# Performance work log

Measured on AMD Instinct MI355X. Metric: run time of the kernel, lower is better.

Reference implementation:

```python
import jax, jax.numpy as jnp
import numpy as np

N_USERS = 50000
N_ITEMS = 50000
N = N_USERS + N_ITEMS
DIM = 64
N_LAYERS = 3
N_EDGES = 1250000
BN_EPS = 1e-5


def setup_inputs() -> dict:
    key = jax.random.key(0)
    k_x, k_e, k_w, k_b = jax.random.split(key, 4)
    x = jax.random.normal(k_x, (N, DIM), dtype=jnp.float32)
    edge_index = jax.random.randint(k_e, (2, N_EDGES), 0, N, dtype=jnp.int64)
    # Glorot-ish init for the per-layer GCNConv linear weights [L, DIM, DIM]
    Ws = jax.random.normal(k_w, (N_LAYERS, DIM, DIM), dtype=jnp.float32) * (1.0 / np.sqrt(DIM))
    bs = jnp.zeros((N_LAYERS, DIM), dtype=jnp.float32)
    gamma = jnp.ones((DIM,), dtype=jnp.float32)
    beta = jnp.zeros((DIM,), dtype=jnp.float32)
    return {"x": x, "edge_index": edge_index, "Ws": Ws, "bs": bs,
            "gamma": gamma, "beta": beta}


def _gcn_conv(x, W, b, src, dst, deg_inv_sqrt):
    # PyG GCNConv: h = x @ W^T ; out_i = sum_{j->i} norm_ji * h_j + b
    h = x @ W.T                                   # [N, DIM]
    norm = deg_inv_sqrt[src] * deg_inv_sqrt[dst]  # [E2]
    msg = h[src] * norm[:, None]                  # gather over irregular edges
    out = jax.ops.segment_sum(msg, dst, num_segments=N)
    return out + b


def reference(x, edge_index, Ws, bs, gamma, beta):
    # Add self-loops once (same augmented graph for every layer).
    loops = jnp.arange(N, dtype=edge_index.dtype)
    src = jnp.concatenate([edge_index[0], loops])  # source nodes j
    dst = jnp.concatenate([edge_index[1], loops])  # target nodes i
    # Symmetric normalization degrees (edge weight 1, counted at targets).
    deg = jax.ops.segment_sum(jnp.ones_like(dst, dtype=x.dtype), dst, num_segments=N)
    deg_inv_sqrt = jnp.where(deg > 0, jax.lax.rsqrt(deg), 0.0)

    for i in range(N_LAYERS):
        x = _gcn_conv(x, Ws[i], bs[i], src, dst, deg_inv_sqrt)

    # BatchNorm1d (training-mode batch statistics, biased variance)
    mean = jnp.mean(x, axis=0)
    var = jnp.mean((x - mean) ** 2, axis=0)
    x = (x - mean) * jax.lax.rsqrt(var + BN_EPS) * gamma + beta

    users, items = x[:N_USERS], x[N_USERS:]
    return users, items
```

## Files before the change

### kernel.cpp

```cpp
#include <hip/hip_runtime.h>

#define NN      100000
#define NUSERS  50000
#define NE      1250000
#define DIM     64
#define BN_EPS  1e-5f
#define NBUCK   8
#define NCHUNK  320
#define SLOT    40

typedef __attribute__((ext_vector_type(8))) short s16x8;
typedef __attribute__((ext_vector_type(4))) float f32x4;

__device__ __forceinline__ short f2b(float f) {
    unsigned u = __builtin_bit_cast(unsigned, f);
    u = (u + 0x7fffu + ((u >> 16) & 1u)) >> 16;
    return (short)u;
}
__device__ __forceinline__ float b2f(unsigned short s) {
    unsigned u = ((unsigned)s) << 16;
    return __builtin_bit_cast(float, u);
}

__global__ __launch_bounds__(256) void place_part(const int* __restrict__ ei,
                                                  int* __restrict__ cursor,
                                                  int* __restrict__ csr_src) {
    __shared__ int Qd[4][128];
    __shared__ int Qs[4][128];
    int lane = threadIdx.x & 63, wave = threadIdx.x >> 6;
    int B = blockIdx.x & (NBUCK - 1);
    int gw = (blockIdx.x >> 3) * 4 + wave;
    const int NW  = NCHUNK * 4;
    const int per = (NE + NW - 1) / NW;
    int e0 = gw * per;
    int e1 = e0 + per; if (e1 > NE) e1 = NE;
    int qn = 0;
    for (int e = e0 + lane; e - lane < e1; e += 64) {
        bool keep = false; int d = 0, s = 0;
        if (e < e1) {
            d = __builtin_nontemporal_load(&ei[NE + e]);
            keep = ((d / 12500) == B);
            if (keep) s = __builtin_nontemporal_load(&ei[e]);
        }
        unsigned long long m = __ballot(keep);
        if (keep) {
            int rank = __popcll(m & ((1ull << lane) - 1ull));
            Qd[wave][qn + rank] = d;
            Qs[wave][qn + rank] = s;
        }
        qn += __popcll(m);
        if (qn >= 64) {
            int dd = Qd[wave][lane];
            int ss = Qs[wave][lane];
            int pos = atomicAdd(&cursor[dd], 1);
            if (pos < SLOT) csr_src[dd * SLOT + pos] = ss;
            qn -= 64;
            int mvd = (lane < qn) ? Qd[wave][64 + lane] : 0;
            int mvs = (lane < qn) ? Qs[wave][64 + lane] : 0;
            if (lane < qn) { Qd[wave][lane] = mvd; Qs[wave][lane] = mvs; }
        }
    }
    if (lane < qn) {
        int dd = Qd[wave][lane];
        int pos = atomicAdd(&cursor[dd], 1);
        if (pos < SLOT) csr_src[dd * SLOT + pos] = Qs[wave][lane];
    }
}

__global__ __launch_bounds__(256) void dinv_kernel(const int* __restrict__ cursor,
                                                   float* __restrict__ dinv) {
    int v = blockIdx.x * blockDim.x + threadIdx.x;
    if (v < NN) dinv[v] = rsqrtf((float)cursor[v] + 1.0f);
}

__global__ __launch_bounds__(128) void c0_kernel(const float* __restrict__ Ws,
                                                 const float* __restrict__ bs,
                                                 float* __restrict__ c0) {
    int t = threadIdx.x;
    if (t < 128) {
        int l = t >> 6, j = t & 63;
        const float* Wl = Ws + (size_t)(l + 1) * 4096;
        const float* bl = bs + l * 64;
        float s = 0.0f;
        for (int k = 0; k < 64; ++k) s += bl[k] * Wl[j * 64 + k];
        c0[t] = s;
    }
}

template <int L0>
__global__ __launch_bounds__(256) void gemm_mfma(const void* __restrict__ Xin,
                                                 const float* __restrict__ W,
                                                 const float* __restrict__ dinv,
                                                 const float* __restrict__ c0,
                                                 unsigned short* __restrict__ Gb) {
    int lane = threadIdx.x & 63;
    int n16 = lane & 15, quad = lane >> 4;

    s16x8 bfrag[4][2];
#pragma unroll
    for (int t = 0; t < 4; ++t)
#pragma unroll
        for (int c = 0; c < 2; ++c) {
            const float4* wp = (const float4*)(W + (t * 16 + n16) * 64 + c * 32 + quad * 8);
            float4 w0 = wp[0], w1 = wp[1];
            s16x8 f;
            f[0] = f2b(w0.x); f[1] = f2b(w0.y); f[2] = f2b(w0.z); f[3] = f2b(w0.w);
            f[4] = f2b(w1.x); f[5] = f2b(w1.y); f[6] = f2b(w1.z); f[7] = f2b(w1.w);
            bfrag[t][c] = f;
        }

    int wid = (blockIdx.x * blockDim.x + threadIdx.x) >> 6;
    int nw  = (gridDim.x * blockDim.x) >> 6;
    for (int tile = wid; tile < NN / 16; tile += nw) {
        int r0 = tile * 16;
        int m  = r0 + n16;
        s16x8 a[2];
#pragma unroll
        for (int c = 0; c < 2; ++c) {
            if (L0) {
                const float4* xp = (const float4*)((const float*)Xin + (size_t)m * 64 + c * 32 + quad * 8);
                float4 x0 = xp[0], x1 = xp[1];
                s16x8 f;
                f[0] = f2b(x0.x); f[1] = f2b(x0.y); f[2] = f2b(x0.z); f[3] = f2b(x0.w);
                f[4] = f2b(x1.x); f[5] = f2b(x1.y); f[6] = f2b(x1.z); f[7] = f2b(x1.w);
                a[c] = f;
            } else {
                a[c] = *(const s16x8*)((const unsigned short*)Xin + (size_t)m * 64 + c * 32 + quad * 8);
            }
        }
        f32x4 acc[4] = {{0,0,0,0},{0,0,0,0},{0,0,0,0},{0,0,0,0}};
#pragma unroll
        for (int c = 0; c < 2; ++c)
#pragma unroll
            for (int t = 0; t < 4; ++t)
                acc[t] = __builtin_amdgcn_mfma_f32_16x16x32_bf16(a[c], bfrag[t][c], acc[t], 0, 0, 0);

        float dvr[4];
#pragma unroll
        for (int r = 0; r < 4; ++r) dvr[r] = dinv[r0 + quad * 4 + r];
#pragma unroll
        for (int t = 0; t < 4; ++t) {
            float cc = L0 ? 0.0f : c0[t * 16 + n16];
#pragma unroll
            for (int r = 0; r < 4; ++r) {
                float dv = dvr[r];
                float g  = L0 ? dv * acc[t][r] : dv * dv * acc[t][r] + dv * cc;
                Gb[(size_t)(r0 + quad * 4 + r) * 64 + t * 16 + n16] = (unsigned short)f2b(g);
            }
        }
    }
}

__global__ __launch_bounds__(256) void gather_b(const int* __restrict__ cursor,
                                                const int* __restrict__ csr_src,
                                                const unsigned short* __restrict__ Gb,
                                                unsigned short* __restrict__ ACCb) {
    int lane = threadIdx.x & 63;
    int c = lane & 15, g = lane >> 4;
    int wid  = (blockIdx.x * blockDim.x + threadIdx.x) >> 6;
    int nw   = (gridDim.x * blockDim.x) >> 6;
    for (int v = wid * 2; v < NN; v += nw * 2) {
        int w = v + 1;
        int n0 = cursor[v]; if (n0 > SLOT) n0 = SLOT;
        int n1 = cursor[w]; if (n1 > SLOT) n1 = SLOT;
        float m0 = (g == 0) ? 1.0f : 0.0f;
        float a0x, a0y, a0z, a0w, a1x, a1y, a1z, a1w;
        {
            ushort4 s0 = *(const ushort4*)(Gb + (size_t)v * 64 + c * 4);
            ushort4 s1 = *(const ushort4*)(Gb + (size_t)w * 64 + c * 4);
            a0x = m0 * b2f(s0.x); a0y = m0 * b2f(s0.y);
            a0z = m0 * b2f(s0.z); a0w = m0 * b2f(s0.w);
            a1x = m0 * b2f(s1.x); a1y = m0 * b2f(s1.y);
            a1z = m0 * b2f(s1.z); a1w = m0 * b2f(s1.w);
        }
        int idx0 = (lane < n0) ? csr_src[v * SLOT + lane] : 0;
        int idx1 = (lane < n1) ? csr_src[w * SLOT + lane] : 0;
        int nmax = (n0 > n1) ? n0 : n1;
        for (int t = 0; t < nmax; t += 16) {
            ushort4 val0[4], val1[4];
            float msk0[4], msk1[4];
#pragma unroll
            for (int u = 0; u < 4; ++u) {
                int nb = t + u * 4 + g;
                int s0 = __shfl(idx0, nb & 63, 64);
                int s1 = __shfl(idx1, nb & 63, 64);
                bool ok0 = nb < n0, ok1 = nb < n1;
                msk0[u] = ok0 ? 1.0f : 0.0f;
                msk1[u] = ok1 ? 1.0f : 0.0f;
                val0[u] = *(const ushort4*)(Gb + (size_t)(ok0 ? s0 : v) * 64 + c * 4);
                val1[u] = *(const ushort4*)(Gb + (size_t)(ok1 ? s1 : w) * 64 + c * 4);
            }
#pragma unroll
            for (int u = 0; u < 4; ++u) {
                a0x = fmaf(msk0[u], b2f(val0[u].x), a0x);
                a0y = fmaf(msk0[u], b2f(val0[u].y), a0y);
                a0z = fmaf(msk0[u], b2f(val0[u].z), a0z);
                a0w = fmaf(msk0[u], b2f(val0[u].w), a0w);
                a1x = fmaf(msk1[u], b2f(val1[u].x), a1x);
                a1y = fmaf(msk1[u], b2f(val1[u].y), a1y);
                a1z = fmaf(msk1[u], b2f(val1[u].z), a1z);
                a1w = fmaf(msk1[u], b2f(val1[u].w), a1w);
            }
        }
#pragma unroll
        for (int off = 16; off < 64; off <<= 1) {
            a0x += __shfl_xor(a0x, off, 64); a0y += __shfl_xor(a0y, off, 64);
            a0z += __shfl_xor(a0z, off, 64); a0w += __shfl_xor(a0w, off, 64);
            a1x += __shfl_xor(a1x, off, 64); a1y += __shfl_xor(a1y, off, 64);
            a1z += __shfl_xor(a1z, off, 64); a1w += __shfl_xor(a1w, off, 64);
        }
        if (g == 0) {
            ushort4 o0, o1;
            o0.x = (unsigned short)f2b(a0x); o0.y = (unsigned short)f2b(a0y);
            o0.z = (unsigned short)f2b(a0z); o0.w = (unsigned short)f2b(a0w);
            o1.x = (unsigned short)f2b(a1x); o1.y = (unsigned short)f2b(a1y);
            o1.z = (unsigned short)f2b(a1z); o1.w = (unsigned short)f2b(a1w);
            *(ushort4*)(ACCb + (size_t)v * 64 + c * 4) = o0;
            *(ushort4*)(ACCb + (size_t)w * 64 + c * 4) = o1;
        }
    }
}

__global__ __launch_bounds__(256) void bn_stats(const unsigned short* __restrict__ ACCb,
                                                const float* __restrict__ dinv,
                                                const float* __restrict__ blast,
                                                float* __restrict__ sums) {
    int j = threadIdx.x & 63;
    float b = blast[j];
    int wid = (blockIdx.x * blockDim.x + threadIdx.x) >> 6;
    int nw  = (gridDim.x * blockDim.x) >> 6;
    float s = 0.0f, s2 = 0.0f;
    for (int v = wid; v < NN; v += nw) {
        float y = dinv[v] * b2f(ACCb[(size_t)v * 64 + j]) + b;
        s += y;
        s2 += y * y;
    }
    __shared__ float ls[256], ls2[256];
    ls[threadIdx.x] = s;
    ls2[threadIdx.x] = s2;
    __syncthreads();
    if (threadIdx.x < 64) {
        s  = ls[threadIdx.x] + ls[threadIdx.x + 64] + ls[threadIdx.x + 128] + ls[threadIdx.x + 192];
        s2 = ls2[threadIdx.x] + ls2[threadIdx.x + 64] + ls2[threadIdx.x + 128] + ls2[threadIdx.x + 192];
        atomicAdd(&sums[j], s);
        atomicAdd(&sums[64 + j], s2);
    }
}

__global__ __launch_bounds__(256) void bn_apply(const unsigned short* __restrict__ ACCb,
                                                const float* __restrict__ dinv,
                                                const float* __restrict__ blast,
                                                const float* __restrict__ sums,
                                                const float* __restrict__ gamma,
                                                const float* __restrict__ beta,
                                                float* __restrict__ out) {
    const float invN = 1.0f / (float)NN;
    int stride = gridDim.x * blockDim.x;
    for (int i = blockIdx.x * blockDim.x + threadIdx.x; i < NN * 64; i += stride) {
        int j = i & 63;
        int v = i >> 6;
        float mean = sums[j] * invN;
        float var  = sums[64 + j] * invN - mean * mean;
        float y = dinv[v] * b2f(ACCb[i]) + blast[j];
        out[i] = (y - mean) * rsqrtf(var + BN_EPS) * gamma[j] + beta[j];
    }
}

extern "C" void kernel_launch(void* const* d_in, const int* in_sizes, int n_in,
                              void* d_out, int out_size, void* d_ws, size_t ws_size,
                              hipStream_t stream) {
    const float* x     = (const float*)d_in[0];
    const int*   ei    = (const int*)d_in[1];
    const float* Ws    = (const float*)d_in[2];
    const float* bs    = (const float*)d_in[3];
    const float* gamma = (const float*)d_in[4];
    const float* beta  = (const float*)d_in[5];
    float* out = (float*)d_out;

    char* ws = (char*)d_ws;
    size_t off = 0;
    unsigned short* ACCb = (unsigned short*)(ws + off); off += (size_t)NN * 64 * 2;
    unsigned short* Gb   = (unsigned short*)(ws + off); off += (size_t)NN * 64 * 2;
    float* dinv    = (float*)(ws + off); off += (size_t)NN * 4;
    float* sums    = (float*)(ws + off); off += 128 * 4;
    float* c0      = (float*)(ws + off); off += 128 * 4;
    int*   cursor  = (int*)(ws + off);   off += (size_t)NN * 4;
    int*   csr_src = (int*)(ws + off);   off += (size_t)NN * SLOT * 4;

    hipMemsetAsync(cursor, 0, NN * sizeof(int), stream);
    hipMemsetAsync(sums, 0, 128 * sizeof(float), stream);

    place_part<<<NBUCK * NCHUNK, 256, 0, stream>>>(ei, cursor, csr_src);
    dinv_kernel<<<(NN + 255) / 256, 256, 0, stream>>>(cursor, dinv);
    c0_kernel<<<1, 128, 0, stream>>>(Ws, bs, c0);

    gemm_mfma<1><<<1563, 256, 0, stream>>>(x, Ws, dinv, nullptr, Gb);
    gather_b<<<3072, 256, 0, stream>>>(cursor, csr_src, Gb, ACCb);
    for (int l = 1; l < 3; ++l) {
        gemm_mfma<0><<<1563, 256, 0, stream>>>(ACCb, Ws + (size_t)l * 4096, dinv,
                                               c0 + (l - 1) * 64, Gb);
        gather_b<<<3072, 256, 0, stream>>>(cursor, csr_src, Gb, ACCb);
    }

    bn_stats<<<2048, 256, 0, stream>>>(ACCb, dinv, bs + 128, sums);
    bn_apply<<<2048, 256, 0, stream>>>(ACCb, dinv, bs + 128, sums, gamma, beta, out);
}
```

Baseline: 380.7 us.

## Split gather by column quarter across blocks and fuse BN stats into last gather

The gather kernel now assigns each group of 8 blocks to four 16-column quarters of the feature row. Each lane loads 4 columns, and 16 neighbour groups per wave walk the edge list. Blocks sharing a quarter touch the same slice of Gb, which may improve cache locality. The column-statistics pass of the batch norm is fused into the last gather through shared-memory and global atomics, removing one full read of ACCb. The cost is more index shuffles per edge, redundant csr and cursor reads across quarters, and shared atomic contention.

```diff
diff --git a/kernel.cpp b/kernel.cpp
--- a/kernel.cpp
+++ b/kernel.cpp
@@ -151,99 +151,95 @@
     }
 }
 
-__global__ __launch_bounds__(256) void gather_b(const int* __restrict__ cursor,
+template <int FUSE>
+__global__ __launch_bounds__(256) void gather_q(const int* __restrict__ cursor,
                                                 const int* __restrict__ csr_src,
                                                 const unsigned short* __restrict__ Gb,
-                                                unsigned short* __restrict__ ACCb) {
-    int lane = threadIdx.x & 63;
-    int c = lane & 15, g = lane >> 4;
-    int wid  = (blockIdx.x * blockDim.x + threadIdx.x) >> 6;
-    int nw   = (gridDim.x * blockDim.x) >> 6;
-    for (int v = wid * 2; v < NN; v += nw * 2) {
+                                                unsigned short* __restrict__ ACCb,
+                                                const float* __restrict__ dinv,
+                                                const float* __restrict__ blast,
+                                                float* __restrict__ sums) {
+    __shared__ float bsum[16], bsum2[16];
+    int lane = threadIdx.x & 63, wave = threadIdx.x >> 6;
+    int r = blockIdx.x & 7;
+    int q = r >> 1, sub = r & 1;
+    int bq  = (blockIdx.x >> 3) * 2 + sub;
+    int wid = bq * 4 + wave;
+    int nwq = ((gridDim.x >> 3) * 2) * 4;
+    int c4 = lane & 3, g = lane >> 2;
+    int colbase = q * 16 + c4 * 4;
+
+    if (FUSE) {
+        if (threadIdx.x < 16) { bsum[threadIdx.x] = 0.0f; bsum2[threadIdx.x] = 0.0f; }
+        __syncthreads();
+    }
+
+    float mg0 = (g == 0) ? 1.0f : 0.0f;
+    for (int v = wid * 2; v < NN; v += nwq * 2) {
         int w = v + 1;
         int n0 = cursor[v]; if (n0 > SLOT) n0 = SLOT;
         int n1 = cursor[w]; if (n1 > SLOT) n1 = SLOT;
-        float m0 = (g == 0) ? 1.0f : 0.0f;
-        float a0x, a0y, a0z, a0w, a1x, a1y, a1z, a1w;
+        float a0[4], a1[4];
         {
-            ushort4 s0 = *(const ushort4*)(Gb + (size_t)v * 64 + c * 4);
-            ushort4 s1 = *(const ushort4*)(Gb + (size_t)w * 64 + c * 4);
-            a0x = m0 * b2f(s0.x); a0y = m0 * b2f(s0.y);
-            a0z = m0 * b2f(s0.z); a0w = m0 * b2f(s0.w);
-            a1x = m0 * b2f(s1.x); a1y = m0 * b2f(s1.y);
-            a1z = m0 * b2f(s1.z); a1w = m0 * b2f(s1.w);
+            ushort4 s0 = *(const ushort4*)(Gb + (size_t)v * 64 + colbase);
+            ushort4 s1 = *(const ushort4*)(Gb + (size_t)w * 64 + colbase);
+            a0[0] = mg0 * b2f(s0.x); a0[1] = mg0 * b2f(s0.y);
+            a0[2] = mg0 * b2f(s0.z); a0[3] = mg0 * b2f(s0.w);
+            a1[0] = mg0 * b2f(s1.x); a1[1] = mg0 * b2f(s1.y);
+            a1[2] = mg0 * b2f(s1.z); a1[3] = mg0 * b2f(s1.w);
         }
         int idx0 = (lane < n0) ? csr_src[v * SLOT + lane] : 0;
         int idx1 = (lane < n1) ? csr_src[w * SLOT + lane] : 0;
         int nmax = (n0 > n1) ? n0 : n1;
         for (int t = 0; t < nmax; t += 16) {
-            ushort4 val0[4], val1[4];
-            float msk0[4], msk1[4];
-#pragma unroll
-            for (int u = 0; u < 4; ++u) {
-                int nb = t + u * 4 + g;
-                int s0 = __shfl(idx0, nb & 63, 64);
-                int s1 = __shfl(idx1, nb & 63, 64);
-                bool ok0 = nb < n0, ok1 = nb < n1;
-                msk0[u] = ok0 ? 1.0f : 0.0f;
-                msk1[u] = ok1 ? 1.0f : 0.0f;
-                val0[u] = *(const ushort4*)(Gb + (size_t)(ok0 ? s0 : v) * 64 + c * 4);
-                val1[u] = *(const ushort4*)(Gb + (size_t)(ok1 ? s1 : w) * 64 + c * 4);
+            int nb = t + g;
+            int s0 = __shfl(idx0, nb & 63, 64);
+            int s1 = __shfl(idx1, nb & 63, 64);
+            bool ok0 = nb < n0, ok1 = nb < n1;
+            float k0 = ok0 ? 1.0f : 0.0f;
+            float k1 = ok1 ? 1.0f : 0.0f;
+            ushort4 u0 = *(const ushort4*)(Gb + (size_t)(ok0 ? s0 : v) * 64 + colbase);
+            ushort4 u1 = *(const ushort4*)(Gb + (size_t)(ok1 ? s1 : w) * 64 + colbase);
+            a0[0] = fmaf(k0, b2f(u0.x), a0[0]); a0[1] = fmaf(k0, b2f(u0.y), a0[1]);
+            a0[2] = fmaf(k0, b2f(u0.z), a0[2]); a0[3] = fmaf(k0, b2f(u0.w), a0[3]);
+            a1[0] = fmaf(k1, b2f(u1.x), a1[0]); a1[1] = fmaf(k1, b2f(u1.y), a1[1]);
+            a1[2] = fmaf(k1, b2f(u1.z), a1[2]); a1[3] = fmaf(k1, b2f(u1.w), a1[3]);
+        }
+#pragma unroll
+        for (int off = 4; off < 64; off <<= 1) {
+#pragma unroll
+            for (int k = 0; k < 4; ++k) {
+                a0[k] += __shfl_xor(a0[k], off, 64);
+                a1[k] += __shfl_xor(a1[k], off, 64);
             }
-#pragma unroll
-            for (int u = 0; u < 4; ++u) {
-                a0x = fmaf(msk0[u], b2f(val0[u].x), a0x);
-                a0y = fmaf(msk0[u], b2f(val0[u].y), a0y);
-                a0z = fmaf(msk0[u], b2f(val0[u].z), a0z);
-                a0w = fmaf(msk0[u], b2f(val0[u].w), a0w);
-                a1x = fmaf(msk1[u], b2f(val1[u].x), a1x);
-                a1y = fmaf(msk1[u], b2f(val1[u].y), a1y);
-                a1z = fmaf(msk1[u], b2f(val1[u].z), a1z);
-                a1w = fmaf(msk1[u], b2f(val1[u].w), a1w);
-            }
-        }
-#pragma unroll
-        for (int off = 16; off < 64; off <<= 1) {
-            a0x += __shfl_xor(a0x, off, 64); a0y += __shfl_xor(a0y, off, 64);
-            a0z += __shfl_xor(a0z, off, 64); a0w += __shfl_xor(a0w, off, 64);
-            a1x += __shfl_xor(a1x, off, 64); a1y += __shfl_xor(a1y, off, 64);
-            a1z += __shfl_xor(a1z, off, 64); a1w += __shfl_xor(a1w, off, 64);
         }
         if (g == 0) {
             ushort4 o0, o1;
-            o0.x = (unsigned short)f2b(a0x); o0.y = (unsigned short)f2b(a0y);
-            o0.z = (unsigned short)f2b(a0z); o0.w = (unsigned short)f2b(a0w);
-            o1.x = (unsigned short)f2b(a1x); o1.y = (unsigned short)f2b(a1y);
-            o1.z = (unsigned short)f2b(a1z); o1.w = (unsigned short)f2b(a1w);
-            *(ushort4*)(ACCb + (size_t)v * 64 + c * 4) = o0;
-            *(ushort4*)(ACCb + (size_t)w * 64 + c * 4) = o1;
-        }
-    }
-}
-
-__global__ __launch_bounds__(256) void bn_stats(const unsigned short* __restrict__ ACCb,
-                                                const float* __restrict__ dinv,
-                                                const float* __restrict__ blast,
-                                                float* __restrict__ sums) {
-    int j = threadIdx.x & 63;
-    float b = blast[j];
-    int wid = (blockIdx.x * blockDim.x + threadIdx.x) >> 6;
-    int nw  = (gridDim.x * blockDim.x) >> 6;
-    float s = 0.0f, s2 = 0.0f;
-    for (int v = wid; v < NN; v += nw) {
-        float y = dinv[v] * b2f(ACCb[(size_t)v * 64 + j]) + b;
-        s += y;
-        s2 += y * y;
-    }
-    __shared__ float ls[256], ls2[256];
-    ls[threadIdx.x] = s;
-    ls2[threadIdx.x] = s2;
-    __syncthreads();
-    if (threadIdx.x < 64) {
-        s  = ls[threadIdx.x] + ls[threadIdx.x + 64] + ls[threadIdx.x + 128] + ls[threadIdx.x + 192];
-        s2 = ls2[threadIdx.x] + ls2[threadIdx.x + 64] + ls2[threadIdx.x + 128] + ls2[threadIdx.x + 192];
-        atomicAdd(&sums[j], s);
-        atomicAdd(&sums[64 + j], s2);
+            o0.x = (unsigned short)f2b(a0[0]); o0.y = (unsigned short)f2b(a0[1]);
+            o0.z = (unsigned short)f2b(a0[2]); o0.w = (unsigned short)f2b(a0[3]);
+            o1.x = (unsigned short)f2b(a1[0]); o1.y = (unsigned short)f2b(a1[1]);
+            o1.z = (unsigned short)f2b(a1[2]); o1.w = (unsigned short)f2b(a1[3]);
+            *(ushort4*)(ACCb + (size_t)v * 64 + colbase) = o0;
+            *(ushort4*)(ACCb + (size_t)w * 64 + colbase) = o1;
+            if (FUSE) {
+                float dv0 = dinv[v], dv1 = dinv[w];
+#pragma unroll
+                for (int k = 0; k < 4; ++k) {
+                    float bl = blast[colbase + k];
+                    float y0 = dv0 * a0[k] + bl;
+                    float y1 = dv1 * a1[k] + bl;
+                    atomicAdd(&bsum[c4 * 4 + k],  y0 + y1);
+                    atomicAdd(&bsum2[c4 * 4 + k], y0 * y0 + y1 * y1);
+                }
+            }
+        }
+    }
+    if (FUSE) {
+        __syncthreads();
+        if (threadIdx.x < 16) {
+            atomicAdd(&sums[q * 16 + threadIdx.x],      bsum[threadIdx.x]);
+            atomicAdd(&sums[64 + q * 16 + threadIdx.x], bsum2[threadIdx.x]);
+        }
     }
 }
 
@@ -295,13 +291,14 @@
     c0_kernel<<<1, 128, 0, stream>>>(Ws, bs, c0);
 
     gemm_mfma<1><<<1563, 256, 0, stream>>>(x, Ws, dinv, nullptr, Gb);
-    gather_b<<<3072, 256, 0, stream>>>(cursor, csr_src, Gb, ACCb);
-    for (int l = 1; l < 3; ++l) {
-        gemm_mfma<0><<<1563, 256, 0, stream>>>(ACCb, Ws + (size_t)l * 4096, dinv,
-                                               c0 + (l - 1) * 64, Gb);
-        gather_b<<<3072, 256, 0, stream>>>(cursor, csr_src, Gb, ACCb);
-    }
-
-    bn_stats<<<2048, 256, 0, stream>>>(ACCb, dinv, bs + 128, sums);
+    gather_q<0><<<3072, 256, 0, stream>>>(cursor, csr_src, Gb, ACCb,
+                                          dinv, bs + 128, nullptr);
+    gemm_mfma<0><<<1563, 256, 0, stream>>>(ACCb, Ws + 4096, dinv, c0, Gb);
+    gather_q<0><<<3072, 256, 0, stream>>>(cursor, csr_src, Gb, ACCb,
+                                          dinv, bs + 128, nullptr);
+    gemm_mfma<0><<<1563, 256, 0, stream>>>(ACCb, Ws + 8192, dinv, c0 + 64, Gb);
+    gather_q<1><<<3072, 256, 0, stream>>>(cursor, csr_src, Gb, ACCb,
+                                          dinv, bs + 128, sums);
+
     bn_apply<<<2048, 256, 0, stream>>>(ACCb, dinv, bs + 128, sums, gamma, beta, out);
 }
```

Result: slower. 535.3 us (+40.6%).
